# Optimization experiments

Hardware: AMD Instinct MI355X
Metric: run time of the kernel (lower is better)

Reference implementation:

```python
import jax, jax.numpy as jnp
import numpy as np
import math

N = 1024
C = 128
H = 4
HD = C // H  # 32
HID = C // 2  # geom_mlp hidden


def setup_inputs() -> dict:
    key = jax.random.key(0)
    ks = jax.random.split(key, 12)
    s = 0.02
    return {
        "x": jax.random.normal(ks[0], (N, C), jnp.float32),
        "y": jax.random.normal(ks[1], (N, C), jnp.float32),
        "pos": jax.random.normal(ks[2], (N, 3), jnp.float32),
        "Wq": jax.random.normal(ks[3], (C, C), jnp.float32) * s,
        "bq": jnp.zeros((C,), jnp.float32),
        "Wk": jax.random.normal(ks[4], (C, C), jnp.float32) * s,
        "bk": jnp.zeros((C,), jnp.float32),
        "Wv": jax.random.normal(ks[5], (C, C), jnp.float32) * s,
        "bv": jnp.zeros((C,), jnp.float32),
        "W1": jax.random.normal(ks[6], (3, HID), jnp.float32) * s,
        "b1": jnp.zeros((HID,), jnp.float32),
        "W2": jax.random.normal(ks[7], (HID, C), jnp.float32) * s,
        "b2": jnp.zeros((C,), jnp.float32),
    }


def _safe_norm(sq):
    # sqrt with zero (sub)gradient at 0, matching torch.norm behavior
    pos_mask = sq > 0
    return jnp.where(pos_mask, jnp.sqrt(jnp.where(pos_mask, sq, 1.0)), 0.0)


def reference(x, y, pos, Wq, bq, Wk, bk, Wv, bv, W1, b1, W2, b2):
    # pairwise geometry
    pos_diff = pos[:, None, :] - pos[None, :, :]          # [N, N, 3]
    dist = _safe_norm(jnp.sum(pos_diff * pos_diff, -1))   # [N, N]
    geom = jax.nn.relu(pos_diff @ W1 + b1) @ W2 + b2      # [N, N, C]
    geom = geom.reshape(N, N, H, HD)                      # per-head split

    q = (x @ Wq + bq).reshape(N, H, HD)
    k = (y @ Wk + bk).reshape(N, H, HD)
    v = (y @ Wv + bv).reshape(N, H, HD)

    attn = jnp.einsum("ihd,jhd->hij", q, k) / math.sqrt(HD)  # [H, N, N]
    geom_attn = jnp.einsum("ihd,ijhd->hij", q, geom)         # [H, N, N]
    scores = attn + geom_attn - dist[None, :, :]
    p = jax.nn.softmax(scores, axis=-1)
    out = jnp.einsum("hij,jhd->ihd", p, v).reshape(N, C)     # [N, C]
    return out
```

## Files before the change

### kernel.cpp

```cpp
#include <hip/hip_runtime.h>
#include <math.h>


typedef float v2f __attribute__((ext_vector_type(2)));
typedef float v4f __attribute__((ext_vector_type(4)));

#define L2E 1.4426950408889634f
#define RSL (0.17677669529663687f * L2E)

static __device__ __forceinline__ float dot4(float4 a, float4 b) {
  return a.x*b.x + a.y*b.y + a.z*b.z + a.w*b.w;
}
static __device__ __forceinline__ v2f fma2(v2f a, v2f b, v2f c) {
  return __builtin_elementwise_fma(a, b, c);
}
static __device__ __forceinline__ v4f fma4s(float s, v4f b, v4f c) {
  v4f sv = {s, s, s, s};
  return __builtin_elementwise_fma(sv, b, c);
}

__global__ __launch_bounds__(384) void k_pre(
    const float* __restrict__ x, const float* __restrict__ y, const float* __restrict__ pos,
    const float* __restrict__ Wq, const float* __restrict__ bq,
    const float* __restrict__ Wk, const float* __restrict__ bk,
    const float* __restrict__ Wv, const float* __restrict__ bv,
    const float* __restrict__ W1, const float* __restrict__ b1,
    const float* __restrict__ W2, const float* __restrict__ b2,
    float* __restrict__ q, float* __restrict__ v,
    float* __restrict__ kT4f, float* __restrict__ uT4f,
    float* __restrict__ sA, float* __restrict__ pos4w)
{
  __shared__ float xs[256], ys[256], qs[256];
  __shared__ __align__(16) float4 W2S[64*33];

  const int t  = threadIdx.x;
  const int n0 = blockIdx.x * 2;

  if (t < 256) { xs[t] = x[n0*128 + t]; ys[t] = y[n0*128 + t]; }
  {
    const float4* w2g = (const float4*)W2;
    #pragma unroll
    for (int r = 0; r < 6; ++r) {
      const int e = t + 384*r;
      if (e < 2048) W2S[(e>>5)*33 + (e&31)] = w2g[e];
    }
  }
  __syncthreads();

  {
    const int c   = t & 127;
    const int mat = t >> 7;
    const float* W    = (mat == 0) ? Wq : (mat == 1 ? Wk : Wv);
    const float* S    = (mat == 0) ? xs : ys;
    const float* bias = (mat == 0) ? bq : (mat == 1 ? bk : bv);
    float a0 = 0.f, a1 = 0.f;
    #pragma unroll 8
    for (int d = 0; d < 128; ++d) {
      const float w_ = W[d*128 + c];
      a0 = fmaf(S[d],       w_, a0);
      a1 = fmaf(S[128 + d], w_, a1);
    }
    const float bb = bias[c];
    a0 += bb; a1 += bb;
    if (mat == 0) {
      q[n0*128 + c] = a0 * RSL; q[(n0+1)*128 + c] = a1 * RSL;
      qs[c] = a0; qs[128 + c] = a1;
    } else if (mat == 2) {
      v[n0*128 + c] = a0; v[(n0+1)*128 + c] = a1;
    } else {
      kT4f[((c>>2)*1024 + n0  )*4 + (c&3)] = a0;
      kT4f[((c>>2)*1024 + n0+1)*4 + (c&3)] = a1;
    }
  }
  __syncthreads();

  if (t < 256) {
    const int m = t & 63, h = t >> 6;
    const float4* qs4 = (const float4*)qs;
    #pragma unroll
    for (int ii = 0; ii < 2; ++ii) {
      float acc = 0.f;
      #pragma unroll
      for (int ch = 0; ch < 8; ++ch)
        acc += dot4(qs4[ii*32 + h*8 + ch], W2S[m*33 + h*8 + ch]);
      sA[(n0+ii)*328 + 8 + (m>>2)*20 + h*4 + (m&3)] = acc * L2E;
    }
    if (t < 8) {
      const int ii = t >> 2, h2 = t & 3;
      float ca = 0.f;
      #pragma unroll
      for (int d = 0; d < 32; ++d) ca = fmaf(qs[ii*128 + h2*32 + d], b2[h2*32 + d], ca);
      sA[(n0+ii)*328 + h2] = ca * L2E;
    } else if (t < 16) {
      const int tt = t-8, ii = tt>>2, cc = tt&3;
      sA[(n0+ii)*328 + 4 + cc] = (cc < 3) ? pos[(n0+ii)*3 + cc] * L2E : 0.f;
    } else if (t < 24) {
      const int tt = t-16, ii = tt>>2, cc = tt&3;
      pos4w[(n0+ii)*4 + cc] = (cc < 3) ? pos[(n0+ii)*3 + cc] * L2E : 0.f;
    }
  } else {
    const int tt = t - 256, ii = tt >> 6, m = tt & 63;
    float ua = 0.f;
    #pragma unroll
    for (int cc = 0; cc < 3; ++cc) ua = fmaf(pos[(n0+ii)*3 + cc], W1[cc*64 + m], ua);
    uT4f[((m>>2)*1024 + (n0+ii))*4 + (m&3)] = ua;
    sA[(n0+ii)*328 + 8 + (m>>2)*20 + 16 + (m&3)] = ua + b1[m];
  }
}

__global__ __launch_bounds__(512, 8) void k_attn(
    const float* __restrict__ q, const float* __restrict__ v,
    const v4f* __restrict__ kT4, const v4f* __restrict__ uT4,
    const float* __restrict__ sA, const v4f* __restrict__ pos4,
    float* __restrict__ wsP)
{
  __shared__ __align__(16) float eL[8*544];
  __shared__ __align__(16) float rnum[4096];
  __shared__ float rden[64];

  const int t     = threadIdx.x;
  const int i0    = (blockIdx.x >> 1) * 2;
  const int jhalf = blockIdx.x & 1;
  const int w     = t >> 6;
  const int lane  = t & 63;
  const int c4    = lane & 31;
  const int rep   = lane >> 5;
  const int hh    = c4 >> 3;

  const int jt = jhalf*8 + w;
  const int jb = jt*64;
  const int j  = jb + lane;

  const float* sA0 = sA + i0*328;
  const float* sA1 = sA0 + 328;
  const float* q0  = q + i0*128;
  const float* q1  = q0 + 128;

  const float c00 = sA0[0], c01 = sA0[1], c02 = sA0[2], c03 = sA0[3];
  const float c10 = sA1[0], c11 = sA1[1], c12 = sA1[2], c13 = sA1[3];
  const float p0x = sA0[4], p0y = sA0[5], p0z = sA0[6];
  const float p1x = sA1[4], p1y = sA1[5], p1z = sA1[6];

  const v4f pj = pos4[j];
  const float d0x = p0x-pj.x, d0y = p0y-pj.y, d0z = p0z-pj.z;
  const float d1x = p1x-pj.x, d1y = p1y-pj.y, d1z = p1z-pj.z;
  const float dist0 = sqrtf(d0x*d0x + d0y*d0y + d0z*d0z);
  const float dist1 = sqrtf(d1x*d1x + d1y*d1y + d1z*d1z);

  v2f g0a={0.f,0.f}, g0b={0.f,0.f}, g0c={0.f,0.f}, g0d={0.f,0.f};
  v2f g1a={0.f,0.f}, g1b={0.f,0.f}, g1c={0.f,0.f}, g1d={0.f,0.f};
  #pragma unroll 4
  for (int mb = 0; mb < 16; ++mb) {
    const v4f uj = uT4[mb*1024 + j];
    const v2f uj01 = uj.xy, uj23 = uj.zw;
    const v2f z = {0.f, 0.f};
    {
      const float* ab = sA0 + 8 + mb*20;
      const v2f h01 = __builtin_elementwise_max(*(const v2f*)(ab+16) - uj01, z);
      const v2f h23 = __builtin_elementwise_max(*(const v2f*)(ab+18) - uj23, z);
      g0a = fma2(h01, *(const v2f*)(ab+ 0), g0a); g0a = fma2(h23, *(const v2f*)(ab+ 2), g0a);
      g0b = fma2(h01, *(const v2f*)(ab+ 4), g0b); g0b = fma2(h23, *(const v2f*)(ab+ 6), g0b);
      g0c = fma2(h01, *(const v2f*)(ab+ 8), g0c); g0c = fma2(h23, *(const v2f*)(ab+10), g0c);
      g0d = fma2(h01, *(const v2f*)(ab+12), g0d); g0d = fma2(h23, *(const v2f*)(ab+14), g0d);
    }
    {
      const float* ab = sA1 + 8 + mb*20;
      const v2f h01 = __builtin_elementwise_max(*(const v2f*)(ab+16) - uj01, z);
      const v2f h23 = __builtin_elementwise_max(*(const v2f*)(ab+18) - uj23, z);
      g1a = fma2(h01, *(const v2f*)(ab+ 0), g1a); g1a = fma2(h23, *(const v2f*)(ab+ 2), g1a);
      g1b = fma2(h01, *(const v2f*)(ab+ 4), g1b); g1b = fma2(h23, *(const v2f*)(ab+ 6), g1b);
      g1c = fma2(h01, *(const v2f*)(ab+ 8), g1c); g1c = fma2(h23, *(const v2f*)(ab+10), g1c);
      g1d = fma2(h01, *(const v2f*)(ab+12), g1d); g1d = fma2(h23, *(const v2f*)(ab+14), g1d);
    }
  }

  v2f s0a={0.f,0.f}, s0b={0.f,0.f}, s0c={0.f,0.f}, s0d={0.f,0.f};
  v2f s1a={0.f,0.f}, s1b={0.f,0.f}, s1c={0.f,0.f}, s1d={0.f,0.f};
  #pragma unroll 8
  for (int cb = 0; cb < 8; ++cb) {
    const v4f k0 = kT4[(cb     )*1024 + j];
    const v4f k1 = kT4[(cb +  8)*1024 + j];
    const v4f k2 = kT4[(cb + 16)*1024 + j];
    const v4f k3 = kT4[(cb + 24)*1024 + j];
    s0a = fma2(k0.xy, *(const v2f*)(q0 + cb*4      ), s0a); s0a = fma2(k0.zw, *(const v2f*)(q0 + cb*4 +  2), s0a);
    s0b = fma2(k1.xy, *(const v2f*)(q0 + cb*4 + 32 ), s0b); s0b = fma2(k1.zw, *(const v2f*)(q0 + cb*4 + 34), s0b);
    s0c = fma2(k2.xy, *(const v2f*)(q0 + cb*4 + 64 ), s0c); s0c = fma2(k2.zw, *(const v2f*)(q0 + cb*4 + 66), s0c);
    s0d = fma2(k3.xy, *(const v2f*)(q0 + cb*4 + 96 ), s0d); s0d = fma2(k3.zw, *(const v2f*)(q0 + cb*4 + 98), s0d);
    s1a = fma2(k0.xy, *(const v2f*)(q1 + cb*4      ), s1a); s1a = fma2(k0.zw, *(const v2f*)(q1 + cb*4 +  2), s1a);
    s1b = fma2(k1.xy, *(const v2f*)(q1 + cb*4 + 32 ), s1b); s1b = fma2(k1.zw, *(const v2f*)(q1 + cb*4 + 34), s1b);
    s1c = fma2(k2.xy, *(const v2f*)(q1 + cb*4 + 64 ), s1c); s1c = fma2(k2.zw, *(const v2f*)(q1 + cb*4 + 66), s1c);
    s1d = fma2(k3.xy, *(const v2f*)(q1 + cb*4 + 96 ), s1d); s1d = fma2(k3.zw, *(const v2f*)(q1 + cb*4 + 98), s1d);
  }

  float lsum[8];
  float* eW = &eL[w*544];
  {
    const v2f t0a = s0a + g0a, t0b = s0b + g0b, t0c = s0c + g0c, t0d = s0d + g0d;
    const float p0 = exp2f(t0a.x + t0a.y + (c00 - dist0));
    const float p1 = exp2f(t0b.x + t0b.y + (c01 - dist0));
    const float p2 = exp2f(t0c.x + t0c.y + (c02 - dist0));
    const float p3 = exp2f(t0d.x + t0d.y + (c03 - dist0));
    lsum[0] = p0; lsum[1] = p1; lsum[2] = p2; lsum[3] = p3;
    eW[      lane] = p0; eW[ 68 + lane] = p1; eW[136 + lane] = p2; eW[204 + lane] = p3;
    const v2f t1a = s1a + g1a, t1b = s1b + g1b, t1c = s1c + g1c, t1d = s1d + g1d;
    const float r0 = exp2f(t1a.x + t1a.y + (c10 - dist1));
    const float r1 = exp2f(t1b.x + t1b.y + (c11 - dist1));
    const float r2 = exp2f(t1c.x + t1c.y + (c12 - dist1));
    const float r3 = exp2f(t1d.x + t1d.y + (c13 - dist1));
    lsum[4] = r0; lsum[5] = r1; lsum[6] = r2; lsum[7] = r3;
    eW[272 + lane] = r0; eW[340 + lane] = r1; eW[408 + lane] = r2; eW[476 + lane] = r3;
  }
  __builtin_amdgcn_wave_barrier();

  v4f acc0 = {0.f,0.f,0.f,0.f};
  v4f acc1 = {0.f,0.f,0.f,0.f};
  {
    const v4f* er0 = (const v4f*)&eL[w*544 +  hh    *68 + rep*32];
    const v4f* er1 = (const v4f*)&eL[w*544 + (4+hh) *68 + rep*32];
    const v4f* vg = (const v4f*)(v + jb*128);
    const int vbase = rep*32*32 + c4;
    #pragma unroll 4
    for (int jj4 = 0; jj4 < 8; ++jj4) {
      const v4f e0 = er0[jj4];
      const v4f e1 = er1[jj4];
      const v4f va = vg[vbase + (jj4*4+0)*32];
      const v4f vb = vg[vbase + (jj4*4+1)*32];
      const v4f vc = vg[vbase + (jj4*4+2)*32];
      const v4f vd = vg[vbase + (jj4*4+3)*32];
      acc0 = fma4s(e0.x, va, acc0); acc1 = fma4s(e1.x, va, acc1);
      acc0 = fma4s(e0.y, vb, acc0); acc1 = fma4s(e1.y, vb, acc1);
      acc0 = fma4s(e0.z, vc, acc0); acc1 = fma4s(e1.z, vc, acc1);
      acc0 = fma4s(e0.w, vd, acc0); acc1 = fma4s(e1.w, vd, acc1);
    }
  }
  __builtin_amdgcn_wave_barrier();

  #pragma unroll
  for (int mm = 1; mm < 64; mm <<= 1) {
    #pragma unroll
    for (int r8 = 0; r8 < 8; ++r8) lsum[r8] += __shfl_xor(lsum[r8], mm);
  }
  ((v4f*)rnum)[((w*2+0)*2 + rep)*32 + c4] = acc0;
  ((v4f*)rnum)[((w*2+1)*2 + rep)*32 + c4] = acc1;
  if (lane == 0) {
    #pragma unroll
    for (int r8 = 0; r8 < 8; ++r8) rden[w*8 + r8] = lsum[r8];
  }
  __syncthreads();

  float* P = wsP + (size_t)blockIdx.x * 264;
  if (t < 256) {
    const int ii = t >> 7, c = t & 127;
    float num = 0.f;
    #pragma unroll
    for (int ww = 0; ww < 8; ++ww) {
      num += rnum[((ww*2+ii)*2+0)*128 + c];
      num += rnum[((ww*2+ii)*2+1)*128 + c];
    }
    P[ii*128 + c] = num;
  }
  if (t >= 256 && t < 264) {
    const int r8 = t - 256;
    float den = 0.f;
    #pragma unroll
    for (int ww = 0; ww < 8; ++ww) den += rden[ww*8 + r8];
    P[256 + r8] = den;
  }
}

__global__ __launch_bounds__(512) void k_fin(const float* __restrict__ wsP,
                                             float* __restrict__ out)
{
  const int gid = blockIdx.x * 512 + threadIdx.x;
  const int i = gid >> 7, c = gid & 127;
  const int ipair = i >> 1, ii = i & 1;
  const float* P0 = wsP + (size_t)(ipair*2+0) * 264;
  const float* P1 = wsP + (size_t)(ipair*2+1) * 264;
  const float num = P0[ii*128 + c] + P1[ii*128 + c];
  const float den = P0[256 + ii*4 + (c>>5)] + P1[256 + ii*4 + (c>>5)];
  out[gid] = num / den;
}

extern "C" void kernel_launch(void* const* d_in, const int* in_sizes, int n_in,
                              void* d_out, int out_size, void* d_ws, size_t ws_size,
                              hipStream_t stream) {
  const float* x   = (const float*)d_in[0];
  const float* y   = (const float*)d_in[1];
  const float* pos = (const float*)d_in[2];
  const float* Wq  = (const float*)d_in[3];
  const float* bq  = (const float*)d_in[4];
  const float* Wk  = (const float*)d_in[5];
  const float* bk  = (const float*)d_in[6];
  const float* Wv  = (const float*)d_in[7];
  const float* bv  = (const float*)d_in[8];
  const float* W1  = (const float*)d_in[9];
  const float* b1  = (const float*)d_in[10];
  const float* W2  = (const float*)d_in[11];
  const float* b2  = (const float*)d_in[12];

  float* ws = (float*)d_ws;
  float* q    = ws;
  float* v    = ws + 131072;
  float* kT4f = ws + 262144;
  float* uT4f = ws + 393216;
  float* sA   = ws + 458752;
  float* pos4 = ws + 794624;
  float* wsP  = ws + 798720;
  float* out  = (float*)d_out;

  k_pre<<<dim3(512), dim3(384), 0, stream>>>(x, y, pos, Wq, bq, Wk, bk, Wv, bv,
                                             W1, b1, W2, b2,
                                             q, v, kT4f, uT4f, sA, pos4);
  k_attn<<<dim3(1024), dim3(512), 0, stream>>>(q, v, (const v4f*)kT4f,
                                               (const v4f*)uT4f, sA,
                                               (const v4f*)pos4, wsP);
  k_fin<<<dim3(256), dim3(512), 0, stream>>>(wsP, out);
}
```

Before: 120.0 us.

## Fuse final normalization into attention kernel via atomics and last-block flag

```diff
diff --git a/kernel.cpp b/kernel.cpp
--- a/kernel.cpp
+++ b/kernel.cpp
@@ -19,7 +19,7 @@
   return __builtin_elementwise_fma(sv, b, c);
 }
 
-__global__ __launch_bounds__(384) void k_pre(
+__global__ __launch_bounds__(512) void k_pre(
     const float* __restrict__ x, const float* __restrict__ y, const float* __restrict__ pos,
     const float* __restrict__ Wq, const float* __restrict__ bq,
     const float* __restrict__ Wk, const float* __restrict__ bk,
@@ -28,83 +28,103 @@
     const float* __restrict__ W2, const float* __restrict__ b2,
     float* __restrict__ q, float* __restrict__ v,
     float* __restrict__ kT4f, float* __restrict__ uT4f,
-    float* __restrict__ sA, float* __restrict__ pos4w)
+    float* __restrict__ sA, float* __restrict__ pos4w,
+    float* __restrict__ Acc, int* __restrict__ flags)
 {
-  __shared__ float xs[256], ys[256], qs[256];
+  __shared__ float qs[1024];
   __shared__ __align__(16) float4 W2S[64*33];
 
   const int t  = threadIdx.x;
-  const int n0 = blockIdx.x * 2;
-
-  if (t < 256) { xs[t] = x[n0*128 + t]; ys[t] = y[n0*128 + t]; }
+  const int n0 = blockIdx.x * 8;
+
+  for (int e = t; e < 1056; e += 512) Acc[blockIdx.x*1056 + e] = 0.f;
   {
     const float4* w2g = (const float4*)W2;
     #pragma unroll
-    for (int r = 0; r < 6; ++r) {
-      const int e = t + 384*r;
-      if (e < 2048) W2S[(e>>5)*33 + (e&31)] = w2g[e];
-    }
-  }
-  __syncthreads();
-
-  {
-    const int c   = t & 127;
-    const int mat = t >> 7;
+    for (int r = 0; r < 4; ++r) {
+      const int e = t + 512*r;
+      W2S[(e>>5)*33 + (e&31)] = w2g[e];
+    }
+  }
+
+  const int c   = t & 127;
+  const int mat = t >> 7;
+  if (mat < 3) {
     const float* W    = (mat == 0) ? Wq : (mat == 1 ? Wk : Wv);
-    const float* S    = (mat == 0) ? xs : ys;
+    const float* X    = (mat == 0) ? x  : y;
     const float* bias = (mat == 0) ? bq : (mat == 1 ? bk : bv);
-    float a0 = 0.f, a1 = 0.f;
+    float a[8] = {0.f,0.f,0.f,0.f,0.f,0.f,0.f,0.f};
     #pragma unroll 8
     for (int d = 0; d < 128; ++d) {
       const float w_ = W[d*128 + c];
-      a0 = fmaf(S[d],       w_, a0);
-      a1 = fmaf(S[128 + d], w_, a1);
+      #pragma unroll
+      for (int r = 0; r < 8; ++r)
+        a[r] = fmaf(X[(n0+r)*128 + d], w_, a[r]);
     }
     const float bb = bias[c];
-    a0 += bb; a1 += bb;
     if (mat == 0) {
-      q[n0*128 + c] = a0 * RSL; q[(n0+1)*128 + c] = a1 * RSL;
-      qs[c] = a0; qs[128 + c] = a1;
-    } else if (mat == 2) {
-      v[n0*128 + c] = a0; v[(n0+1)*128 + c] = a1;
+      #pragma unroll
+      for (int r = 0; r < 8; ++r) {
+        const float qv = a[r] + bb;
+        q[(n0+r)*128 + c] = qv * RSL;
+        qs[r*128 + c] = qv;
+      }
+    } else if (mat == 1) {
+      #pragma unroll
+      for (int r = 0; r < 8; ++r)
+        kT4f[((c>>2)*1024 + n0+r)*4 + (c&3)] = a[r] + bb;
     } else {
-      kT4f[((c>>2)*1024 + n0  )*4 + (c&3)] = a0;
-      kT4f[((c>>2)*1024 + n0+1)*4 + (c&3)] = a1;
+      #pragma unroll
+      for (int r = 0; r < 8; ++r)
+        v[(n0+r)*128 + c] = a[r] + bb;
+    }
+  } else {
+    const int tt = t - 384;
+    const int m  = tt & 63;
+    const int rh = tt >> 6;
+    #pragma unroll
+    for (int rr = 0; rr < 4; ++rr) {
+      const int r = rh*4 + rr;
+      float ua = 0.f;
+      #pragma unroll
+      for (int cc = 0; cc < 3; ++cc)
+        ua = fmaf(pos[(n0+r)*3 + cc], W1[cc*64 + m], ua);
+      uT4f[((m>>2)*1024 + (n0+r))*4 + (m&3)] = ua;
+      sA[(n0+r)*328 + 8 + (m>>2)*20 + 16 + (m&3)] = ua + b1[m];
+    }
+    if (tt < 32) {
+      const int r = tt >> 2, cm = tt & 3;
+      pos4w[(n0+r)*4 + cm] = (cm < 3) ? pos[(n0+r)*3 + cm] * L2E : 0.f;
+    } else if (tt < 36) {
+      flags[blockIdx.x*4 + (tt-32)] = 0;
     }
   }
   __syncthreads();
 
-  if (t < 256) {
-    const int m = t & 63, h = t >> 6;
+  {
+    const int m = t & 63, h = (t >> 6) & 3, rg = t >> 8;
     const float4* qs4 = (const float4*)qs;
-    #pragma unroll
-    for (int ii = 0; ii < 2; ++ii) {
+    float4 w2c[8];
+    #pragma unroll
+    for (int ch = 0; ch < 8; ++ch) w2c[ch] = W2S[m*33 + h*8 + ch];
+    #pragma unroll
+    for (int rr = 0; rr < 4; ++rr) {
+      const int r = rg + rr*2;
       float acc = 0.f;
       #pragma unroll
-      for (int ch = 0; ch < 8; ++ch)
-        acc += dot4(qs4[ii*32 + h*8 + ch], W2S[m*33 + h*8 + ch]);
-      sA[(n0+ii)*328 + 8 + (m>>2)*20 + h*4 + (m&3)] = acc * L2E;
-    }
-    if (t < 8) {
-      const int ii = t >> 2, h2 = t & 3;
-      float ca = 0.f;
-      #pragma unroll
-      for (int d = 0; d < 32; ++d) ca = fmaf(qs[ii*128 + h2*32 + d], b2[h2*32 + d], ca);
-      sA[(n0+ii)*328 + h2] = ca * L2E;
-    } else if (t < 16) {
-      const int tt = t-8, ii = tt>>2, cc = tt&3;
-      sA[(n0+ii)*328 + 4 + cc] = (cc < 3) ? pos[(n0+ii)*3 + cc] * L2E : 0.f;
-    } else if (t < 24) {
-      const int tt = t-16, ii = tt>>2, cc = tt&3;
-      pos4w[(n0+ii)*4 + cc] = (cc < 3) ? pos[(n0+ii)*3 + cc] * L2E : 0.f;
-    }
-  } else {
-    const int tt = t - 256, ii = tt >> 6, m = tt & 63;
-    float ua = 0.f;
-    #pragma unroll
-    for (int cc = 0; cc < 3; ++cc) ua = fmaf(pos[(n0+ii)*3 + cc], W1[cc*64 + m], ua);
-    uT4f[((m>>2)*1024 + (n0+ii))*4 + (m&3)] = ua;
-    sA[(n0+ii)*328 + 8 + (m>>2)*20 + 16 + (m&3)] = ua + b1[m];
+      for (int ch = 0; ch < 8; ++ch) acc += dot4(qs4[r*32 + h*8 + ch], w2c[ch]);
+      sA[(n0+r)*328 + 8 + (m>>2)*20 + h*4 + (m&3)] = acc * L2E;
+    }
+  }
+  if (t < 32) {
+    const int r = t >> 2, h2 = t & 3;
+    float ca = 0.f;
+    #pragma unroll
+    for (int d = 0; d < 32; ++d) ca = fmaf(qs[r*128 + h2*32 + d], b2[h2*32 + d], ca);
+    sA[(n0+r)*328 + h2] = ca * L2E;
+  } else if (t < 64) {
+    const int tt2 = t - 32, r = tt2 >> 2, cc = tt2 & 3;
+    sA[(n0+r)*328 + 4 + cc] = (cc < 3) ? pos[(n0+r)*3 + cc] * L2E : 0.f;
   }
 }
 
@@ -112,14 +132,18 @@
     const float* __restrict__ q, const float* __restrict__ v,
     const v4f* __restrict__ kT4, const v4f* __restrict__ uT4,
     const float* __restrict__ sA, const v4f* __restrict__ pos4,
-    float* __restrict__ wsP)
+    float* __restrict__ Acc, int* __restrict__ flags,
+    float* __restrict__ out)
 {
   __shared__ __align__(16) float eL[8*544];
   __shared__ __align__(16) float rnum[4096];
   __shared__ float rden[64];
+  __shared__ float denS[8];
+  __shared__ int isLast;
 
   const int t     = threadIdx.x;
-  const int i0    = (blockIdx.x >> 1) * 2;
+  const int ipair = blockIdx.x >> 1;
+  const int i0    = ipair * 2;
   const int jhalf = blockIdx.x & 1;
   const int w     = t >> 6;
   const int lane  = t & 63;
@@ -248,7 +272,7 @@
   }
   __syncthreads();
 
-  float* P = wsP + (size_t)blockIdx.x * 264;
+  float* A = Acc + (size_t)ipair * 264;
   if (t < 256) {
     const int ii = t >> 7, c = t & 127;
     float num = 0.f;
@@ -257,28 +281,29 @@
       num += rnum[((ww*2+ii)*2+0)*128 + c];
       num += rnum[((ww*2+ii)*2+1)*128 + c];
     }
-    P[ii*128 + c] = num;
-  }
-  if (t >= 256 && t < 264) {
+    atomicAdd(&A[t], num);
+  } else if (t < 264) {
     const int r8 = t - 256;
     float den = 0.f;
     #pragma unroll
     for (int ww = 0; ww < 8; ++ww) den += rden[ww*8 + r8];
-    P[256 + r8] = den;
-  }
-}
-
-__global__ __launch_bounds__(512) void k_fin(const float* __restrict__ wsP,
-                                             float* __restrict__ out)
-{
-  const int gid = blockIdx.x * 512 + threadIdx.x;
-  const int i = gid >> 7, c = gid & 127;
-  const int ipair = i >> 1, ii = i & 1;
-  const float* P0 = wsP + (size_t)(ipair*2+0) * 264;
-  const float* P1 = wsP + (size_t)(ipair*2+1) * 264;
-  const float num = P0[ii*128 + c] + P1[ii*128 + c];
-  const float den = P0[256 + ii*4 + (c>>5)] + P1[256 + ii*4 + (c>>5)];
-  out[gid] = num / den;
+    atomicAdd(&A[256 + r8], den);
+  }
+  __syncthreads();
+  __threadfence();
+  if (t == 0) isLast = (atomicAdd(&flags[ipair], 1) == 1);
+  __syncthreads();
+
+  if (isLast) {
+    float numv = 0.f;
+    if (t < 256) numv = atomicAdd(&A[t], 0.f);
+    else if (t < 264) denS[t-256] = atomicAdd(&A[t], 0.f);
+    __syncthreads();
+    if (t < 256) {
+      const int ii = t >> 7, c = t & 127;
+      out[(i0+ii)*128 + c] = numv / denS[ii*4 + (c>>5)];
+    }
+  }
 }
 
 extern "C" void kernel_launch(void* const* d_in, const int* in_sizes, int n_in,
@@ -305,14 +330,15 @@
   float* uT4f = ws + 393216;
   float* sA   = ws + 458752;
   float* pos4 = ws + 794624;
-  float* wsP  = ws + 798720;
+  float* Acc  = ws + 798720;
+  int*   flags= (int*)(ws + 933888);
   float* out  = (float*)d_out;
 
-  k_pre<<<dim3(512), dim3(384), 0, stream>>>(x, y, pos, Wq, bq, Wk, bk, Wv, bv,
+  k_pre<<<dim3(128), dim3(512), 0, stream>>>(x, y, pos, Wq, bq, Wk, bk, Wv, bv,
                                              W1, b1, W2, b2,
-                                             q, v, kT4f, uT4f, sA, pos4);
+                                             q, v, kT4f, uT4f, sA, pos4,
+                                             Acc, flags);
   k_attn<<<dim3(1024), dim3(512), 0, stream>>>(q, v, (const v4f*)kT4f,
                                                (const v4f*)uT4f, sA,
-                                               (const v4f*)pos4, wsP);
-  k_fin<<<dim3(256), dim3(512), 0, stream>>>(wsP, out);
-}
+                                               (const v4f*)pos4, Acc, flags, out);
+}
```

Measured after the change: 249.8 us. 108% more time.
